# Kernel optimization log

Measured on AMD Instinct MI355X. Metric: run time of the kernel, lower is better.

The kernel has to match this reference:

```python
import jax, jax.numpy as jnp
import numpy as np


def _conv1x1(x, w, b):
    # x: [B,Cin,H,W], w: [Cout,Cin], b: [Cout]
    return jnp.einsum('bchw,oc->bohw', x, w) + b[None, :, None, None]


def setup_inputs() -> dict:
    key = jax.random.key(0)
    ks = jax.random.split(key, 9)
    C, Cb = 256, 128
    B, H, W = 8, 32, 32
    s_in = 1.0 / np.sqrt(C)
    s_bn = 1.0 / np.sqrt(Cb)
    return {
        'x': jax.random.normal(ks[0], (B, C, H, W), dtype=jnp.float32),
        'theta_w': jax.random.uniform(ks[1], (Cb, C), jnp.float32, -s_in, s_in),
        'theta_b': jax.random.uniform(ks[2], (Cb,), jnp.float32, -s_in, s_in),
        'phi_w': jax.random.uniform(ks[3], (Cb, C), jnp.float32, -s_in, s_in),
        'phi_b': jax.random.uniform(ks[4], (Cb,), jnp.float32, -s_in, s_in),
        'g_w': jax.random.uniform(ks[5], (Cb, C), jnp.float32, -s_in, s_in),
        'g_b': jax.random.uniform(ks[6], (Cb,), jnp.float32, -s_in, s_in),
        'W_w': jax.random.uniform(ks[7], (C, Cb), jnp.float32, -s_bn, s_bn),
        'W_b': jax.random.uniform(ks[8], (C,), jnp.float32, -s_bn, s_bn),
    }


def reference(x, theta_w, theta_b, phi_w, phi_b, g_w, g_b, W_w, W_b):
    B, C, H, Wd = x.shape
    Cb = theta_w.shape[0]
    theta = _conv1x1(x, theta_w, theta_b).reshape(-1, Cb)      # [N, Cb] (row-major, as torch)
    phi = _conv1x1(x, phi_w, phi_b).reshape(Cb, -1)            # [Cb, N]
    g = _conv1x1(x, g_w, g_b).reshape(-1, Cb)                  # [N, Cb]
    attn = jax.nn.softmax(theta @ phi, axis=1)                 # [N, N] global attention
    out = (attn @ g).reshape(B, -1, H, Wd)                     # [B, Cb, H, W]
    return _conv1x1(out, W_w, W_b) + x
```

## Files before the change

### kernel.cpp

```cpp
#include <hip/hip_runtime.h>

typedef unsigned short u16;
typedef __attribute__((ext_vector_type(8))) short short8;
typedef __attribute__((ext_vector_type(4))) float f32x4;

__device__ __forceinline__ u16 f2bf(float f){
  union { float f; unsigned u; } v; v.f = f;
  unsigned u = v.u;
  u += 0x7fffu + ((u >> 16) & 1u);
  return (u16)(u >> 16);
}

__global__ __launch_bounds__(256) void proj3_kernel(
    const float* __restrict__ x,
    const float* __restrict__ tw, const float* __restrict__ tb,
    const float* __restrict__ pw, const float* __restrict__ pb,
    const float* __restrict__ gw, const float* __restrict__ gb,
    u16* __restrict__ T, u16* __restrict__ PHI, u16* __restrict__ G)
{
  const int proj = blockIdx.y >> 1;
  const int co0  = (blockIdx.y & 1) * 64;
  const float* __restrict__ W    = (proj==0) ? tw : ((proj==1) ? pw : gw);
  const float* __restrict__ bias = (proj==0) ? tb : ((proj==1) ? pb : gb);
  u16* __restrict__ out          = (proj==0) ? T  : ((proj==1) ? PHI : G);
  const int b   = blockIdx.z;
  const int hw0 = blockIdx.x * 64;
  const float* srcb = x + (size_t)b * 262144;

  __shared__ float xs[16][64];
  __shared__ float wT[16][64];
  const int t = threadIdx.x;
  const int tc = t >> 4, th = t & 15;

  float acc[4][4];
  #pragma unroll
  for (int i=0;i<4;i++)
    #pragma unroll
    for (int j=0;j<4;j++) acc[i][j] = 0.f;

  for (int k0 = 0; k0 < 256; k0 += 16){
    __syncthreads();
    {
      int kk = t >> 4, col = (t & 15) * 4;
      *(float4*)&xs[kk][col] = *(const float4*)&srcb[(size_t)(k0+kk)*1024 + hw0 + col];
    }
    {
      int c = t >> 2, kk0 = (t & 3) * 4;
      float4 w4 = *(const float4*)&W[(size_t)(co0 + c) * 256 + k0 + kk0];
      wT[kk0+0][c] = w4.x; wT[kk0+1][c] = w4.y;
      wT[kk0+2][c] = w4.z; wT[kk0+3][c] = w4.w;
    }
    __syncthreads();
    #pragma unroll
    for (int kk=0;kk<16;kk++){
      float4 bv = *(const float4*)&xs[kk][th*4];
      float4 av = *(const float4*)&wT[kk][tc*4];
      float a[4]  = {av.x, av.y, av.z, av.w};
      float bb[4] = {bv.x, bv.y, bv.z, bv.w};
      #pragma unroll
      for (int i=0;i<4;i++)
        #pragma unroll
        for (int j=0;j<4;j++)
          acc[i][j] += a[i]*bb[j];
    }
  }
  #pragma unroll
  for (int i=0;i<4;i++){
    int co = co0 + tc*4 + i;
    float bs = bias[co];
    size_t base = ((size_t)b*128 + co)*1024 + hw0 + th*4;
    ushort4 u;
    u.x = f2bf(acc[i][0]+bs); u.y = f2bf(acc[i][1]+bs);
    u.z = f2bf(acc[i][2]+bs); u.w = f2bf(acc[i][3]+bs);
    *(ushort4*)&out[base] = u;
  }
}

__global__ __launch_bounds__(256) void transpose_bf_kernel(
    const u16* __restrict__ src, u16* __restrict__ dst, int R, int C)
{
  __shared__ u16 tile[64][72];
  const int t = threadIdx.x;
  const int c0 = blockIdx.x*64, r0 = blockIdx.y*64;
  {
    int rr = t >> 2, cs = (t & 3) * 16;
    const u16* s = src + (size_t)(r0+rr)*C + c0 + cs;
    uint4 a0 = *(const uint4*)s;
    uint4 a1 = *(const uint4*)(s+8);
    *(uint4*)&tile[rr][cs]   = a0;
    *(uint4*)&tile[rr][cs+8] = a1;
  }
  __syncthreads();
  {
    int cc = t >> 2, rs = (t & 3) * 16;
    __align__(16) u16 tmp[16];
    #pragma unroll
    for (int i=0;i<16;i++) tmp[i] = tile[rs+i][cc];
    u16* d = dst + (size_t)(c0+cc)*R + r0 + rs;
    *(uint4*)d     = *(uint4*)&tmp[0];
    *(uint4*)(d+8) = *(uint4*)&tmp[8];
  }
}

__global__ __launch_bounds__(256, 3) void attn_kernel(
    const u16* __restrict__ Tq, const u16* __restrict__ Kk,
    const u16* __restrict__ Vt, float* __restrict__ Opart,
    float* __restrict__ lpart, int base, int rem)
{
  __shared__ __align__(16) u16 Ks[64][136];
  __shared__ __align__(16) u16 Vs[128][72];
  __shared__ __align__(16) u16 Pall[4][2048];

  const int t = threadIdx.x;
  const int wave = t >> 6, lane = t & 63;
  const int quad = lane >> 4, n16 = lane & 15;
  const int s  = blockIdx.x;
  const int qg = blockIdx.y;
  const int q0 = qg*128 + wave*32;
  u16* Pw = Pall[wave];
  float* Os = Opart + (size_t)s * 1048576;
  float* ls = lpart + (size_t)s * 8192;

  const int ts   = s*base + (s < rem ? s : rem);
  const int ntil = base + (s < rem ? 1 : 0);

  short8 qa[2][4];
  #pragma unroll
  for (int mt=0;mt<2;mt++)
    #pragma unroll
    for (int kc=0;kc<4;kc++)
      qa[mt][kc] = *(const short8*)(Tq + (size_t)(q0 + mt*16 + n16)*128 + kc*32 + quad*8);

  f32x4 o[2][8];
  float lp[2][4];
  #pragma unroll
  for (int mt=0;mt<2;mt++){
    #pragma unroll
    for (int dt=0;dt<8;dt++){ f32x4 z = {0.f,0.f,0.f,0.f}; o[mt][dt] = z; }
    #pragma unroll
    for (int r=0;r<4;r++) lp[mt][r] = 0.f;
  }

  const int krow = t >> 2, kcs = (t & 3) * 32;
  const int vrow = t >> 1, vcs = (t & 1) * 32;

  for (int kt = ts; kt < ts + ntil; kt++){
    const int key0 = kt * 64;
    __syncthreads();
    #pragma unroll
    for (int i=0;i<4;i++)
      *(uint4*)&Ks[krow][kcs + i*8] =
        *(const uint4*)(Kk + (size_t)(key0 + krow)*128 + kcs + i*8);
    #pragma unroll
    for (int i=0;i<4;i++)
      *(uint4*)&Vs[vrow][vcs + i*8] =
        *(const uint4*)(Vt + (size_t)vrow*8192 + key0 + vcs + i*8);
    __syncthreads();

    #pragma unroll
    for (int nt=0; nt<4; nt++){
      short8 kf[4];
      #pragma unroll
      for (int kc=0;kc<4;kc++)
        kf[kc] = *(const short8*)&Ks[nt*16 + n16][kc*32 + quad*8];
      f32x4 s0 = {0.f,0.f,0.f,0.f}, s1 = {0.f,0.f,0.f,0.f};
      #pragma unroll
      for (int kc=0;kc<4;kc++){
        s0 = __builtin_amdgcn_mfma_f32_16x16x32_bf16(qa[0][kc], kf[kc], s0, 0, 0, 0);
        s1 = __builtin_amdgcn_mfma_f32_16x16x32_bf16(qa[1][kc], kf[kc], s1, 0, 0, 0);
      }
      #pragma unroll
      for (int r=0;r<4;r++){
        float p0 = exp2f(s0[r] * 1.4426950408889634f);
        lp[0][r] += p0;
        Pw[(quad*4 + r)*64      + ((nt*16 + n16) ^ (quad<<3))] = f2bf(p0);
        float p1 = exp2f(s1[r] * 1.4426950408889634f);
        lp[1][r] += p1;
        Pw[(16 + quad*4 + r)*64 + ((nt*16 + n16) ^ (quad<<3))] = f2bf(p1);
      }
    }

    __builtin_amdgcn_s_waitcnt(0xC07F);

    #pragma unroll
    for (int kb=0; kb<2; kb++){
      const int psw = kb*32 + ((quad ^ (n16>>2)) << 3);
      short8 pf0 = *(const short8*)(Pw + n16*64        + psw);
      short8 pf1 = *(const short8*)(Pw + (16 + n16)*64 + psw);
      #pragma unroll
      for (int dt=0; dt<8; dt++){
        short8 vfd = *(const short8*)&Vs[dt*16 + n16][kb*32 + quad*8];
        o[0][dt] = __builtin_amdgcn_mfma_f32_16x16x32_bf16(pf0, vfd, o[0][dt], 0, 0, 0);
        o[1][dt] = __builtin_amdgcn_mfma_f32_16x16x32_bf16(pf1, vfd, o[1][dt], 0, 0, 0);
      }
    }
  }

  float l[2][4];
  #pragma unroll
  for (int mt=0;mt<2;mt++)
    #pragma unroll
    for (int r=0;r<4;r++){
      float v = lp[mt][r];
      v += __shfl_xor(v, 1, 64);
      v += __shfl_xor(v, 2, 64);
      v += __shfl_xor(v, 4, 64);
      v += __shfl_xor(v, 8, 64);
      l[mt][r] = v;
    }

  __syncthreads();

  #pragma unroll
  for (int mt=0;mt<2;mt++){
    #pragma unroll
    for (int dt=0;dt<8;dt++)
      #pragma unroll
      for (int r=0;r<4;r++)
        Os[(size_t)(q0 + mt*16 + quad*4 + r)*128 + dt*16 + n16] = o[mt][dt][r];
    if (n16 == 0)
      #pragma unroll
      for (int r=0;r<4;r++) ls[q0 + mt*16 + quad*4 + r] = l[mt][r];
  }
}

__global__ __launch_bounds__(256) void merge_l_kernel(
    const float* __restrict__ lpart, float* __restrict__ linv, int S)
{
  int i = blockIdx.x*256 + threadIdx.x;
  float v = 0.f;
  for (int sp=0; sp<S; sp++) v += lpart[sp*8192 + i];
  linv[i] = 1.0f / v;
}

__global__ __launch_bounds__(256) void final_kernel(
    const float* __restrict__ Ww, const float* __restrict__ Wb,
    const float* __restrict__ Opart, const float* __restrict__ linv, int S,
    const float* __restrict__ x, float* __restrict__ outp)
{
  const int b   = blockIdx.z;
  const int co0 = blockIdx.y * 64;
  const int hw0 = blockIdx.x * 64;

  __shared__ float xs[16][64];
  __shared__ float wT[16][64];
  const int t = threadIdx.x;
  const int tc = t >> 4, th = t & 15;

  float acc[4][4];
  #pragma unroll
  for (int i=0;i<4;i++)
    #pragma unroll
    for (int j=0;j<4;j++) acc[i][j] = 0.f;

  for (int k0 = 0; k0 < 128; k0 += 16){
    __syncthreads();
    {
      int kk = t >> 4, col = (t & 15) * 4;
      size_t gflat = (size_t)b*131072 + (size_t)(k0+kk)*1024 + hw0 + col;
      int row = (int)(gflat >> 7);
      float a0=0.f, a1=0.f, a2=0.f, a3=0.f;
      for (int sp=0; sp<S; sp++){
        float4 v = *(const float4*)&Opart[(size_t)sp*1048576 + gflat];
        a0 += v.x; a1 += v.y; a2 += v.z; a3 += v.w;
      }
      float inv = linv[row];
      xs[kk][col+0] = a0*inv; xs[kk][col+1] = a1*inv;
      xs[kk][col+2] = a2*inv; xs[kk][col+3] = a3*inv;
    }
    {
      int c = t >> 2, kk0 = (t & 3) * 4;
      float4 w4 = *(const float4*)&Ww[(size_t)(co0 + c) * 128 + k0 + kk0];
      wT[kk0+0][c] = w4.x; wT[kk0+1][c] = w4.y;
      wT[kk0+2][c] = w4.z; wT[kk0+3][c] = w4.w;
    }
    __syncthreads();
    #pragma unroll
    for (int kk=0;kk<16;kk++){
      float4 bv = *(const float4*)&xs[kk][th*4];
      float4 av = *(const float4*)&wT[kk][tc*4];
      float a[4]  = {av.x, av.y, av.z, av.w};
      float bb[4] = {bv.x, bv.y, bv.z, bv.w};
      #pragma unroll
      for (int i=0;i<4;i++)
        #pragma unroll
        for (int j=0;j<4;j++)
          acc[i][j] += a[i]*bb[j];
    }
  }
  #pragma unroll
  for (int i=0;i<4;i++){
    int co = co0 + tc*4 + i;
    float bs = Wb[co];
    size_t base = ((size_t)b*256 + co)*1024 + hw0 + th*4;
    float4 xr = *(const float4*)&x[base];
    float4 r;
    r.x = acc[i][0] + bs + xr.x;
    r.y = acc[i][1] + bs + xr.y;
    r.z = acc[i][2] + bs + xr.z;
    r.w = acc[i][3] + bs + xr.w;
    *(float4*)&outp[base] = r;
  }
}

extern "C" void kernel_launch(void* const* d_in, const int* in_sizes, int n_in,
                              void* d_out, int out_size, void* d_ws, size_t ws_size,
                              hipStream_t stream)
{
  (void)in_sizes; (void)n_in; (void)out_size;
  const float* x  = (const float*)d_in[0];
  const float* tw = (const float*)d_in[1];
  const float* tb = (const float*)d_in[2];
  const float* pw = (const float*)d_in[3];
  const float* pb = (const float*)d_in[4];
  const float* gw = (const float*)d_in[5];
  const float* gb = (const float*)d_in[6];
  const float* Ww = (const float*)d_in[7];
  const float* Wb = (const float*)d_in[8];
  float* outp = (float*)d_out;

  char* ws = (char*)d_ws;
  const size_t MB = 1u << 20;
  u16*   Tbf   = (u16*)(ws);
  u16*   PHIbf = (u16*)(ws + 2*MB);
  u16*   Gbf   = (u16*)(ws + 4*MB);
  u16*   Kbf   = (u16*)(ws + 6*MB);
  u16*   VTbf  = (u16*)(ws + 8*MB);

  const int TILES = 128;
  int S;
  if      (ws_size >= 10*MB + 48*MB + 1*MB) S = 12;
  else if (ws_size >= 10*MB + 40*MB + 1*MB) S = 10;
  else if (ws_size >= 10*MB + 32*MB + 1*MB) S = 8;
  else if (ws_size >= 10*MB + 24*MB + 1*MB) S = 6;
  else                                      S = 4;
  int base = TILES / S, rem = TILES % S;
  float* Opart = (float*)(ws + 10*MB);
  float* lpart = (float*)(ws + 2*MB);
  float* linv  = (float*)(ws + 2*MB + 512*1024);

  proj3_kernel<<<dim3(16, 6, 8), 256, 0, stream>>>(x, tw, tb, pw, pb, gw, gb,
                                                   Tbf, PHIbf, Gbf);
  transpose_bf_kernel<<<dim3(128, 2), 256, 0, stream>>>(PHIbf, Kbf, 128, 8192);
  transpose_bf_kernel<<<dim3(2, 128), 256, 0, stream>>>(Gbf, VTbf, 8192, 128);
  attn_kernel<<<dim3(S, 64), 256, 0, stream>>>(Tbf, Kbf, VTbf, Opart, lpart,
                                               base, rem);
  merge_l_kernel<<<dim3(32), 256, 0, stream>>>(lpart, linv, S);
  final_kernel<<<dim3(16, 4, 8), 256, 0, stream>>>(Ww, Wb, Opart, linv, S, x, outp);
}
```

Before: 199.7 us.

## Widen attention query tiles, store bf16 partials, and add a dedicated merge kernel

Each wave in the attention kernel now handles 64 query rows instead of 32, so every K/V fragment read from LDS feeds twice as many MFMAs. The key split is now a fixed 16 or 8 equal-sized chunks, and the grid dimensions are swapped. Partial outputs are written as bf16 in a vectorised, channel-permuted layout rather than scattered fp32 stores. A new merge kernel sums the splits once, normalises by the softmax denominator and writes a bf16 merged tensor, so the final projection no longer re-reads every split. The costs are higher register pressure (occupancy hint lowered from 3 to 2), more rounding error from bf16 partials, and one extra pass over the data.

New measurement: 218.9 us. 1.1x slower.

```diff
diff --git a/kernel.cpp b/kernel.cpp
--- a/kernel.cpp
+++ b/kernel.cpp
@@ -9,6 +9,10 @@
   unsigned u = v.u;
   u += 0x7fffu + ((u >> 16) & 1u);
   return (u16)(u >> 16);
+}
+__device__ __forceinline__ float bf2f(u16 h){
+  union { unsigned u; float f; } v; v.u = ((unsigned)h) << 16;
+  return v.f;
 }
 
 __global__ __launch_bounds__(256) void proj3_kernel(
@@ -102,39 +106,38 @@
   }
 }
 
-__global__ __launch_bounds__(256, 3) void attn_kernel(
+__global__ __launch_bounds__(256, 2) void attn_kernel(
     const u16* __restrict__ Tq, const u16* __restrict__ Kk,
-    const u16* __restrict__ Vt, float* __restrict__ Opart,
-    float* __restrict__ lpart, int base, int rem)
+    const u16* __restrict__ Vt, u16* __restrict__ Opart,
+    float* __restrict__ lpart, int ntil)
 {
   __shared__ __align__(16) u16 Ks[64][136];
   __shared__ __align__(16) u16 Vs[128][72];
-  __shared__ __align__(16) u16 Pall[4][2048];
+  __shared__ __align__(16) u16 Pall[4][4096];
 
   const int t = threadIdx.x;
   const int wave = t >> 6, lane = t & 63;
   const int quad = lane >> 4, n16 = lane & 15;
-  const int s  = blockIdx.x;
-  const int qg = blockIdx.y;
-  const int q0 = qg*128 + wave*32;
+  const int qg = blockIdx.x;
+  const int s  = blockIdx.y;
+  const int q0 = qg*256 + wave*64;
   u16* Pw = Pall[wave];
-  float* Os = Opart + (size_t)s * 1048576;
+  u16*   Os = Opart + (size_t)s * 1048576;
   float* ls = lpart + (size_t)s * 8192;
 
-  const int ts   = s*base + (s < rem ? s : rem);
-  const int ntil = base + (s < rem ? 1 : 0);
-
-  short8 qa[2][4];
-  #pragma unroll
-  for (int mt=0;mt<2;mt++)
+  const int ts = s * ntil;
+
+  short8 qa[4][4];
+  #pragma unroll
+  for (int mt=0;mt<4;mt++)
     #pragma unroll
     for (int kc=0;kc<4;kc++)
       qa[mt][kc] = *(const short8*)(Tq + (size_t)(q0 + mt*16 + n16)*128 + kc*32 + quad*8);
 
-  f32x4 o[2][8];
-  float lp[2][4];
-  #pragma unroll
-  for (int mt=0;mt<2;mt++){
+  f32x4 o[4][8];
+  float lp[4][4];
+  #pragma unroll
+  for (int mt=0;mt<4;mt++){
     #pragma unroll
     for (int dt=0;dt<8;dt++){ f32x4 z = {0.f,0.f,0.f,0.f}; o[mt][dt] = z; }
     #pragma unroll
@@ -163,20 +166,18 @@
       #pragma unroll
       for (int kc=0;kc<4;kc++)
         kf[kc] = *(const short8*)&Ks[nt*16 + n16][kc*32 + quad*8];
-      f32x4 s0 = {0.f,0.f,0.f,0.f}, s1 = {0.f,0.f,0.f,0.f};
-      #pragma unroll
-      for (int kc=0;kc<4;kc++){
-        s0 = __builtin_amdgcn_mfma_f32_16x16x32_bf16(qa[0][kc], kf[kc], s0, 0, 0, 0);
-        s1 = __builtin_amdgcn_mfma_f32_16x16x32_bf16(qa[1][kc], kf[kc], s1, 0, 0, 0);
-      }
-      #pragma unroll
-      for (int r=0;r<4;r++){
-        float p0 = exp2f(s0[r] * 1.4426950408889634f);
-        lp[0][r] += p0;
-        Pw[(quad*4 + r)*64      + ((nt*16 + n16) ^ (quad<<3))] = f2bf(p0);
-        float p1 = exp2f(s1[r] * 1.4426950408889634f);
-        lp[1][r] += p1;
-        Pw[(16 + quad*4 + r)*64 + ((nt*16 + n16) ^ (quad<<3))] = f2bf(p1);
+      #pragma unroll
+      for (int mt=0;mt<4;mt++){
+        f32x4 sa = {0.f,0.f,0.f,0.f};
+        #pragma unroll
+        for (int kc=0;kc<4;kc++)
+          sa = __builtin_amdgcn_mfma_f32_16x16x32_bf16(qa[mt][kc], kf[kc], sa, 0, 0, 0);
+        #pragma unroll
+        for (int r=0;r<4;r++){
+          float pe = exp2f(sa[r] * 1.4426950408889634f);
+          lp[mt][r] += pe;
+          Pw[(mt*16 + quad*4 + r)*64 + ((nt*16 + n16) ^ (quad<<3))] = f2bf(pe);
+        }
       }
     }
 
@@ -185,20 +186,23 @@
     #pragma unroll
     for (int kb=0; kb<2; kb++){
       const int psw = kb*32 + ((quad ^ (n16>>2)) << 3);
-      short8 pf0 = *(const short8*)(Pw + n16*64        + psw);
-      short8 pf1 = *(const short8*)(Pw + (16 + n16)*64 + psw);
+      short8 pf[4];
+      #pragma unroll
+      for (int mt=0;mt<4;mt++)
+        pf[mt] = *(const short8*)(Pw + (mt*16 + n16)*64 + psw);
       #pragma unroll
       for (int dt=0; dt<8; dt++){
         short8 vfd = *(const short8*)&Vs[dt*16 + n16][kb*32 + quad*8];
-        o[0][dt] = __builtin_amdgcn_mfma_f32_16x16x32_bf16(pf0, vfd, o[0][dt], 0, 0, 0);
-        o[1][dt] = __builtin_amdgcn_mfma_f32_16x16x32_bf16(pf1, vfd, o[1][dt], 0, 0, 0);
+        #pragma unroll
+        for (int mt=0;mt<4;mt++)
+          o[mt][dt] = __builtin_amdgcn_mfma_f32_16x16x32_bf16(pf[mt], vfd, o[mt][dt], 0, 0, 0);
       }
     }
   }
 
-  float l[2][4];
-  #pragma unroll
-  for (int mt=0;mt<2;mt++)
+  float l[4][4];
+  #pragma unroll
+  for (int mt=0;mt<4;mt++)
     #pragma unroll
     for (int r=0;r<4;r++){
       float v = lp[mt][r];
@@ -209,34 +213,75 @@
       l[mt][r] = v;
     }
 
+  #pragma unroll
+  for (int mt=0;mt<4;mt++){
+    #pragma unroll
+    for (int r=0;r<4;r++){
+      __align__(16) u16 tmp[8];
+      #pragma unroll
+      for (int dt=0;dt<8;dt++) tmp[dt] = f2bf(o[mt][dt][r]);
+      *(uint4*)(Os + (size_t)(q0 + mt*16 + quad*4 + r)*128 + n16*8) = *(uint4*)tmp;
+    }
+    if (n16 == 0)
+      #pragma unroll
+      for (int r=0;r<4;r++) ls[q0 + mt*16 + quad*4 + r] = l[mt][r];
+  }
+}
+
+__global__ __launch_bounds__(256) void merge_o_kernel(
+    const u16* __restrict__ Opart, const float* __restrict__ lpart, int S,
+    u16* __restrict__ Om)
+{
+  __shared__ u16 Tm[64][136];
+  __shared__ float lrow[64];
+  const int t = threadIdx.x;
+  const int row0 = blockIdx.x * 64;
+
+  if (t < 64){
+    float v = 0.f;
+    for (int sp=0; sp<S; sp++) v += lpart[sp*8192 + row0 + t];
+    lrow[t] = 1.0f / v;
+  }
+
+  const int rl = t >> 2;
+  const int cb = (t & 3) * 32;
+  float acc[32];
+  #pragma unroll
+  for (int j=0;j<32;j++) acc[j] = 0.f;
+  for (int sp=0; sp<S; sp++){
+    const u16* p = Opart + (size_t)sp*1048576 + (size_t)(row0 + rl)*128 + cb;
+    #pragma unroll
+    for (int q=0;q<4;q++){
+      ushort4 v = *(const ushort4*)(p + q*8);
+      ushort4 w = *(const ushort4*)(p + q*8 + 4);
+      acc[q*8+0] += bf2f(v.x); acc[q*8+1] += bf2f(v.y);
+      acc[q*8+2] += bf2f(v.z); acc[q*8+3] += bf2f(v.w);
+      acc[q*8+4] += bf2f(w.x); acc[q*8+5] += bf2f(w.y);
+      acc[q*8+6] += bf2f(w.z); acc[q*8+7] += bf2f(w.w);
+    }
+  }
   __syncthreads();
-
-  #pragma unroll
-  for (int mt=0;mt<2;mt++){
-    #pragma unroll
-    for (int dt=0;dt<8;dt++)
-      #pragma unroll
-      for (int r=0;r<4;r++)
-        Os[(size_t)(q0 + mt*16 + quad*4 + r)*128 + dt*16 + n16] = o[mt][dt][r];
-    if (n16 == 0)
-      #pragma unroll
-      for (int r=0;r<4;r++) ls[q0 + mt*16 + quad*4 + r] = l[mt][r];
-  }
-}
-
-__global__ __launch_bounds__(256) void merge_l_kernel(
-    const float* __restrict__ lpart, float* __restrict__ linv, int S)
-{
-  int i = blockIdx.x*256 + threadIdx.x;
-  float v = 0.f;
-  for (int sp=0; sp<S; sp++) v += lpart[sp*8192 + i];
-  linv[i] = 1.0f / v;
+  const float inv = lrow[rl];
+  #pragma unroll
+  for (int j=0;j<32;j++){
+    int cp = cb + j;
+    int ch = (cp & 7)*16 + (cp >> 3);
+    Tm[rl][ch] = f2bf(acc[j] * inv);
+  }
+  __syncthreads();
+  {
+    const int row = t >> 2, seg = (t & 3) * 32;
+    u16* d = Om + (size_t)(row0 + row)*128 + seg;
+    #pragma unroll
+    for (int q=0;q<4;q++)
+      *(uint4*)(d + q*8) = *(const uint4*)&Tm[row][seg + q*8];
+  }
 }
 
 __global__ __launch_bounds__(256) void final_kernel(
     const float* __restrict__ Ww, const float* __restrict__ Wb,
-    const float* __restrict__ Opart, const float* __restrict__ linv, int S,
-    const float* __restrict__ x, float* __restrict__ outp)
+    const u16* __restrict__ Om, const float* __restrict__ x,
+    float* __restrict__ outp)
 {
   const int b   = blockIdx.z;
   const int co0 = blockIdx.y * 64;
@@ -258,15 +303,9 @@
     {
       int kk = t >> 4, col = (t & 15) * 4;
       size_t gflat = (size_t)b*131072 + (size_t)(k0+kk)*1024 + hw0 + col;
-      int row = (int)(gflat >> 7);
-      float a0=0.f, a1=0.f, a2=0.f, a3=0.f;
-      for (int sp=0; sp<S; sp++){
-        float4 v = *(const float4*)&Opart[(size_t)sp*1048576 + gflat];
-        a0 += v.x; a1 += v.y; a2 += v.z; a3 += v.w;
-      }
-      float inv = linv[row];
-      xs[kk][col+0] = a0*inv; xs[kk][col+1] = a1*inv;
-      xs[kk][col+2] = a2*inv; xs[kk][col+3] = a3*inv;
+      ushort4 v = *(const ushort4*)&Om[gflat];
+      xs[kk][col+0] = bf2f(v.x); xs[kk][col+1] = bf2f(v.y);
+      xs[kk][col+2] = bf2f(v.z); xs[kk][col+3] = bf2f(v.w);
     }
     {
       int c = t >> 2, kk0 = (t & 3) * 4;
@@ -328,23 +367,17 @@
   u16*   VTbf  = (u16*)(ws + 8*MB);
 
   const int TILES = 128;
-  int S;
-  if      (ws_size >= 10*MB + 48*MB + 1*MB) S = 12;
-  else if (ws_size >= 10*MB + 40*MB + 1*MB) S = 10;
-  else if (ws_size >= 10*MB + 32*MB + 1*MB) S = 8;
-  else if (ws_size >= 10*MB + 24*MB + 1*MB) S = 6;
-  else                                      S = 4;
-  int base = TILES / S, rem = TILES % S;
-  float* Opart = (float*)(ws + 10*MB);
+  int S = (ws_size >= 10*MB + 32*MB + 1*MB) ? 16 : 8;
+  int ntil = TILES / S;
+  u16*   Opart = (u16*)(ws + 10*MB);
   float* lpart = (float*)(ws + 2*MB);
-  float* linv  = (float*)(ws + 2*MB + 512*1024);
+  u16*   Om    = (u16*)(ws + 4*MB);
 
   proj3_kernel<<<dim3(16, 6, 8), 256, 0, stream>>>(x, tw, tb, pw, pb, gw, gb,
                                                    Tbf, PHIbf, Gbf);
   transpose_bf_kernel<<<dim3(128, 2), 256, 0, stream>>>(PHIbf, Kbf, 128, 8192);
   transpose_bf_kernel<<<dim3(2, 128), 256, 0, stream>>>(Gbf, VTbf, 8192, 128);
-  attn_kernel<<<dim3(S, 64), 256, 0, stream>>>(Tbf, Kbf, VTbf, Opart, lpart,
-                                               base, rem);
-  merge_l_kernel<<<dim3(32), 256, 0, stream>>>(lpart, linv, S);
-  final_kernel<<<dim3(16, 4, 8), 256, 0, stream>>>(Ww, Wb, Opart, linv, S, x, outp);
-}
+  attn_kernel<<<dim3(32, S), 256, 0, stream>>>(Tbf, Kbf, VTbf, Opart, lpart, ntil);
+  merge_o_kernel<<<dim3(128), 256, 0, stream>>>(Opart, lpart, S, Om);
+  final_kernel<<<dim3(16, 4, 8), 256, 0, stream>>>(Ww, Wb, Om, x, outp);
+}
```
